# Optimization experiments

Hardware: AMD Instinct MI355X
Metric: run time of the kernel (lower is better)

## Reference

```python
import jax, jax.numpy as jnp
import numpy as np

HEADS = 4

def _proj(x, w, b):
    # 1x1 conv == per-pixel linear: x [B,C,H,W], w [O,C], b [O]
    return jnp.einsum('oc,bchw->bohw', w, x) + b[None, :, None, None]

def setup_inputs() -> dict:
    key = jax.random.key(0)
    ks = jax.random.split(key, 9)
    B, C, H, W = 16, 512, 32, 32
    emb = C // HEADS
    return {
        'x': jax.random.normal(ks[0], (B, C, H, W), jnp.float32),
        'wq_w': jax.random.normal(ks[1], (C, C), jnp.float32) * 0.02,
        'wq_b': jax.random.normal(ks[2], (C,), jnp.float32) * 0.02,
        'wk_w': jax.random.normal(ks[3], (C, C), jnp.float32) * 0.02,
        'wk_b': jax.random.normal(ks[4], (C,), jnp.float32) * 0.02,
        'wv_w': jax.random.normal(ks[5], (C, C), jnp.float32) * 0.02,
        'wv_b': jax.random.normal(ks[6], (C,), jnp.float32) * 0.02,
        'rh': jax.random.normal(ks[7], (1, HEADS, emb, 1, H), jnp.float32),
        'rw': jax.random.normal(ks[8], (1, HEADS, emb, W, 1), jnp.float32),
    }

def reference(x, wq_w, wq_b, wk_w, wk_b, wv_w, wv_b, rh, rw):
    B, C, H, W = x.shape
    heads = HEADS
    emb = C // heads
    scale = C ** (-0.5)
    N = H * W
    q = _proj(x, wq_w, wq_b).reshape(B, heads, emb, N).transpose(0, 1, 3, 2) * scale  # [B,h,N,d]
    kt = _proj(x, wk_w, wk_b).reshape(B, heads, emb, N)                               # [B,h,d,N]
    v = _proj(x, wv_w, wv_b).reshape(B, heads, emb, N).transpose(0, 1, 3, 2)          # [B,h,N,d]
    qkt = jnp.matmul(q, kt)                                                           # [B,h,N,N]
    # relative-position term: (rh + rw) broadcasts to [1,h,d,W,H], flattened as in source
    rt = (rh + rw).reshape(1, heads, emb, N)
    qrt = jnp.matmul(q, rt)                                                           # [B,h,N,N]
    attn = jax.nn.softmax(qkt + qrt, axis=-1)
    y = jnp.matmul(attn, v)                                                           # [B,h,N,d]
    return y.reshape(B, C, H, W)
```

## Files before the change

### kernel.cpp

```cpp
#include <hip/hip_runtime.h>
#include <hip/hip_bf16.h>
#include <cstdint>

#define NB 16
#define NC 512
#define NPIX 1024
#define NHEADS 4
#define NEMB 128

typedef short bf16x8 __attribute__((ext_vector_type(8)));
typedef float f32x4 __attribute__((ext_vector_type(4)));
typedef float f32x16 __attribute__((ext_vector_type(16)));
typedef unsigned short u16x4 __attribute__((ext_vector_type(4)));
typedef unsigned short u16x8 __attribute__((ext_vector_type(8)));

__device__ __forceinline__ unsigned short f2bf(float f) {
  union { float f; unsigned u; } c; c.f = f;
  return (unsigned short)((c.u + 0x7FFFu + ((c.u >> 16) & 1u)) >> 16);
}

__device__ __forceinline__ unsigned cvtpk_bf16(float lo, float hi) {
  unsigned r;
  asm("v_cvt_pk_bf16_f32 %0, %1, %2" : "=v"(r) : "v"(lo), "v"(hi));
  return r;
}

__device__ __forceinline__ void gload_lds16(const void* g, void* l) {
  __builtin_amdgcn_global_load_lds(
      (const __attribute__((address_space(1))) unsigned int*)g,
      (__attribute__((address_space(3))) unsigned int*)l, 16, 0, 0);
}

__global__ void k_prep_x(const float* __restrict__ x, unsigned short* __restrict__ xt) {
  __shared__ float tile[4][32][33];
  int bid = blockIdx.x;
  int nt = bid & 31, ct4 = (bid >> 5) & 3, b = bid >> 7;
  int n0 = nt * 32, c0 = ct4 * 128;
  int t = threadIdx.x;
  int r = t >> 3, q = t & 7;
#pragma unroll
  for (int s = 0; s < 4; s++) {
    float4 v = *(const float4*)(x + ((size_t)(b * NC + c0 + s * 32 + r)) * NPIX + n0 + q * 4);
    tile[s][r][q * 4 + 0] = v.x; tile[s][r][q * 4 + 1] = v.y;
    tile[s][r][q * 4 + 2] = v.z; tile[s][r][q * 4 + 3] = v.w;
  }
  __syncthreads();
  int cl = q * 4;
#pragma unroll
  for (int s = 0; s < 4; s++) {
    u16x4 o;
    o[0] = f2bf(tile[s][cl + 0][r]); o[1] = f2bf(tile[s][cl + 1][r]);
    o[2] = f2bf(tile[s][cl + 2][r]); o[3] = f2bf(tile[s][cl + 3][r]);
    *(u16x4*)(xt + ((size_t)(b * NPIX + n0 + r)) * NC + c0 + s * 32 + cl) = o;
  }
}

__global__ void k_prep_w(const float* __restrict__ wq, const float* __restrict__ wk,
                         const float* __restrict__ wv, unsigned short* __restrict__ wb) {
  const float* src = blockIdx.y == 0 ? wq : (blockIdx.y == 1 ? wk : wv);
  unsigned short* dst = wb + (size_t)blockIdx.y * NC * NC;
  for (int i = blockIdx.x * 256 + threadIdx.x; i < NC * NC / 4; i += gridDim.x * 256) {
    float4 v = ((const float4*)src)[i];
    u16x4 o = { f2bf(v.x), f2bf(v.y), f2bf(v.z), f2bf(v.w) };
    ((u16x4*)dst)[i] = o;
  }
}

__global__ __launch_bounds__(256, 3) void k_qkv(
    const unsigned short* __restrict__ wb, const unsigned short* __restrict__ xt,
    const float* __restrict__ qb, const float* __restrict__ kb, const float* __restrict__ vb,
    const float* __restrict__ rh, const float* __restrict__ rw,
    unsigned short* __restrict__ Qs, unsigned short* __restrict__ Kn,
    unsigned short* __restrict__ Vm) {
  __shared__ unsigned short Alds[128 * 64];
  __shared__ unsigned short Blds[128 * 64];
  int bid = blockIdx.x;
  int nt = bid & 7, mt = (bid >> 3) & 3;
  int rest = bid >> 5;
  int p = rest % 3, b = rest / 3;
  int m0 = mt * 128, n0 = nt * 128;
  const unsigned short* A = wb + (size_t)p * NC * NC + (size_t)m0 * NC;
  const unsigned short* Bx = xt + (size_t)b * NPIX * NC + (size_t)n0 * NC;
  int t = threadIdx.x;
  int lane = t & 63, wid = t >> 6;
  int wm = (wid >> 1) * 64, wn = (wid & 1) * 64;
  f32x4 acc[4][4] = {};
  for (int k0 = 0; k0 < NC; k0 += 64) {
#pragma unroll
    for (int i = 0; i < 4; i++) {
      int idx = i * 256 + t;
      int row = idx >> 3, col = (idx & 7) * 8;
      gload_lds16(A + (size_t)row * NC + k0 + col, &Alds[idx * 8]);
    }
#pragma unroll
    for (int i = 0; i < 4; i++) {
      int idx = i * 256 + t;
      int row = idx >> 3, col = (idx & 7) * 8;
      gload_lds16(Bx + (size_t)row * NC + k0 + col, &Blds[idx * 8]);
    }
    __syncthreads();
#pragma unroll
    for (int ks = 0; ks < 2; ks++) {
      int kk = ks * 32 + ((lane >> 4) << 3);
      bf16x8 af[4], bfr[4];
#pragma unroll
      for (int f = 0; f < 4; f++)
        af[f] = *(const bf16x8*)&Alds[(wm + f * 16 + (lane & 15)) * 64 + kk];
#pragma unroll
      for (int f = 0; f < 4; f++)
        bfr[f] = *(const bf16x8*)&Blds[(wn + f * 16 + (lane & 15)) * 64 + kk];
#pragma unroll
      for (int fm = 0; fm < 4; fm++)
#pragma unroll
        for (int fn = 0; fn < 4; fn++)
          acc[fm][fn] = __builtin_amdgcn_mfma_f32_16x16x32_bf16(af[fm], bfr[fn], acc[fm][fn], 0, 0, 0);
    }
    __syncthreads();
  }
  const float scale = 0.044194173824159216f * 1.4426950408889634f;
  if (p == 2) {
    unsigned short* vbase = Vm + (size_t)(b * NHEADS + mt) * 131072;
#pragma unroll
    for (int fm = 0; fm < 4; fm++) {
#pragma unroll
      for (int r = 0; r < 4; r++) {
        int d = wm + fm * 16 + ((lane >> 4) << 2) + r;
        float bv = vb[m0 + d];
#pragma unroll
        for (int fn = 0; fn < 4; fn++) {
          int j = n0 + wn + fn * 16 + (lane & 15);
          int tile = j >> 6, jl = j & 63;
          int c2 = jl >> 4, h5 = (jl >> 3) & 1, j8 = jl & 7;
          size_t flat = ((((size_t)tile * 4 + c2) * 2 + h5) * 128 + d) * 8 + j8;
          vbase[flat] = f2bf(acc[fm][fn][r] + bv);
        }
      }
    }
  } else if (p == 1) {
    unsigned short* kbase = Kn + (size_t)(b * NHEADS + mt) * 131072;
#pragma unroll
    for (int fm = 0; fm < 4; fm++) {
      int e0 = wm + fm * 16 + ((lane >> 4) << 2);
      int d8 = e0 >> 4, h5 = (e0 >> 3) & 1, e8 = e0 & 7;
#pragma unroll
      for (int fn = 0; fn < 4; fn++) {
        int j = n0 + wn + fn * 16 + (lane & 15);
        int tile = j >> 6, jl = j & 63;
        u16x4 o;
#pragma unroll
        for (int r = 0; r < 4; r++) {
          float v = acc[fm][fn][r] + kb[m0 + e0 + r];
          v += rh[(m0 + e0 + r) * 32 + (j & 31)] + rw[(m0 + e0 + r) * 32 + (j >> 5)];
          o[r] = f2bf(v);
        }
        size_t flat = ((((size_t)tile * 8 + d8) * 2 + h5) * 64 + jl) * 8 + e8;
        *(u16x4*)(kbase + flat) = o;
      }
    }
  } else {
    unsigned short* dst = Qs + ((size_t)((b * NHEADS + mt) * NPIX + n0)) * NEMB;
#pragma unroll
    for (int fm = 0; fm < 4; fm++) {
      int e0 = wm + fm * 16 + ((lane >> 4) << 2);
#pragma unroll
      for (int fn = 0; fn < 4; fn++) {
        int ncol = wn + fn * 16 + (lane & 15);
        u16x4 o;
#pragma unroll
        for (int r = 0; r < 4; r++)
          o[r] = f2bf((acc[fm][fn][r] + qb[m0 + e0 + r]) * scale);
        *(u16x4*)&dst[(size_t)ncol * NEMB + e0] = o;
      }
    }
  }
}

__global__ __launch_bounds__(256, 2) void k_attn(
    const unsigned short* __restrict__ Qs, const unsigned short* __restrict__ Kp,
    const unsigned short* __restrict__ Vp, float* __restrict__ out) {
  int bid = blockIdx.x;
  int pair = bid & 63;
  int b = pair >> 2, hd = pair & 3;
  int i0 = (bid >> 6) * 128;
  int t = threadIdx.x, w = t >> 6, lane = t & 63;
  int l31 = lane & 31, hi5 = lane >> 5;
  const unsigned short* Qb = Qs + (size_t)pair * NPIX * NEMB;
  const unsigned short* Kg = Kp + (size_t)pair * 131072;
  const unsigned short* Vg = Vp + (size_t)pair * 131072;

  bf16x8 qf[8];
  {
    const unsigned short* qr = Qb + (size_t)(i0 + w * 32 + l31) * NEMB + hi5 * 8;
#pragma unroll
    for (int d8 = 0; d8 < 8; d8++) qf[d8] = *(const bf16x8*)(qr + d8 * 16);
  }
  f32x16 yacc[4] = {};
  float l = 0.f;

  for (int tt = 0; tt < 16; tt++) {
    bf16x8 kf0[8], kf1[8];
#pragma unroll
    for (int d8 = 0; d8 < 8; d8++) {
      const unsigned short* kp = Kg + (((size_t)tt * 8 + d8) * 2 + hi5) * 512;
      kf0[d8] = *(const bf16x8*)(kp + l31 * 8);
      kf1[d8] = *(const bf16x8*)(kp + (l31 + 32) * 8);
    }
    f32x16 sacc[2] = {};
    __builtin_amdgcn_s_setprio(1);
#pragma unroll
    for (int d8 = 0; d8 < 8; d8++) {
      sacc[0] = __builtin_amdgcn_mfma_f32_32x32x16_bf16(kf0[d8], qf[d8], sacc[0], 0, 0, 0);
      sacc[1] = __builtin_amdgcn_mfma_f32_32x32x16_bf16(kf1[d8], qf[d8], sacc[1], 0, 0, 0);
    }
    __builtin_amdgcn_s_setprio(0);
    bf16x8 vf[4][4];
#pragma unroll
    for (int c2 = 0; c2 < 4; c2++)
#pragma unroll
      for (int ds = 0; ds < 4; ds++)
        vf[c2][ds] = *(const bf16x8*)(
            Vg + ((((size_t)tt * 4 + c2) * 2 + hi5) * 128 + ds * 32 + l31) * 8);
    float rs0 = 0.f, rs1 = 0.f, rs2 = 0.f, rs3 = 0.f;
#pragma unroll
    for (int c = 0; c < 2; c++)
#pragma unroll
      for (int i = 0; i < 16; i += 4) {
        float p0 = exp2f(sacc[c][i + 0]);
        float p1 = exp2f(sacc[c][i + 1]);
        float p2 = exp2f(sacc[c][i + 2]);
        float p3 = exp2f(sacc[c][i + 3]);
        sacc[c][i + 0] = p0; sacc[c][i + 1] = p1;
        sacc[c][i + 2] = p2; sacc[c][i + 3] = p3;
        rs0 += p0; rs1 += p1; rs2 += p2; rs3 += p3;
      }
    l += (rs0 + rs1) + (rs2 + rs3);
    unsigned up[2][4][2];
#pragma unroll
    for (int c = 0; c < 2; c++)
#pragma unroll
      for (int g = 0; g < 4; g++) {
        up[c][g][0] = cvtpk_bf16(sacc[c][4 * g + 0], sacc[c][4 * g + 1]);
        up[c][g][1] = cvtpk_bf16(sacc[c][4 * g + 2], sacc[c][4 * g + 3]);
      }
    bf16x8 pf[4];
#pragma unroll
    for (int c2 = 0; c2 < 4; c2++) {
      int c = c2 >> 1, gA = (c2 & 1) * 2, gB = gA + 1;
      unsigned a0 = up[c][gA][0], b0 = up[c][gB][0];
      unsigned a1 = up[c][gA][1], b1 = up[c][gB][1];
      asm("v_permlane32_swap_b32 %0, %1" : "+v"(a0), "+v"(b0));
      asm("v_permlane32_swap_b32 %0, %1" : "+v"(a1), "+v"(b1));
      unsigned wd[4] = { a0, a1, b0, b1 };
      pf[c2] = *(bf16x8*)wd;
    }
    __builtin_amdgcn_s_setprio(1);
#pragma unroll
    for (int c2 = 0; c2 < 4; c2++)
#pragma unroll
      for (int ds = 0; ds < 4; ds++)
        yacc[ds] = __builtin_amdgcn_mfma_f32_32x32x16_bf16(vf[c2][ds], pf[c2], yacc[ds], 0, 0, 0);
    __builtin_amdgcn_s_setprio(0);
  }
  float ltot = l + __shfl_xor(l, 32);
  float invl = 1.0f / ltot;
  int q = i0 + w * 32 + l31;
  float* orow = out + ((size_t)(b * NC + hd * NEMB + (q >> 3))) * NPIX + (q & 7) * NEMB;
#pragma unroll
  for (int ds = 0; ds < 4; ds++)
#pragma unroll
    for (int rg = 0; rg < 4; rg++) {
      f32x4 v;
#pragma unroll
      for (int i = 0; i < 4; i++) v[i] = yacc[ds][rg * 4 + i] * invl;
      *(f32x4*)(orow + ds * 32 + rg * 8 + hi5 * 4) = v;
    }
}

extern "C" void kernel_launch(void* const* d_in, const int* in_sizes, int n_in,
                              void* d_out, int out_size, void* d_ws, size_t ws_size,
                              hipStream_t stream) {
  const float* x  = (const float*)d_in[0];
  const float* wq = (const float*)d_in[1];
  const float* qb = (const float*)d_in[2];
  const float* wk = (const float*)d_in[3];
  const float* kb = (const float*)d_in[4];
  const float* wv = (const float*)d_in[5];
  const float* vb = (const float*)d_in[6];
  const float* rh = (const float*)d_in[7];
  const float* rw = (const float*)d_in[8];
  float* out = (float*)d_out;
  char* ws = (char*)d_ws;
  unsigned short* xt = (unsigned short*)(ws);
  unsigned short* wb = (unsigned short*)(ws + 16777216);
  unsigned short* Q  = (unsigned short*)(ws + 18350080);
  unsigned short* K  = (unsigned short*)(ws + 35127296);
  unsigned short* V  = (unsigned short*)(ws + 51904512);
  k_prep_x<<<2048, 256, 0, stream>>>(x, xt);
  k_prep_w<<<dim3(64, 3), 256, 0, stream>>>(wq, wk, wv, wb);
  k_qkv<<<1536, 256, 0, stream>>>(wb, xt, qb, kb, vb, rh, rw, Q, K, V);
  k_attn<<<512, 256, 0, stream>>>(Q, K, V, out);
}
```

Baseline: 107.6 us.

## Stage K tiles in swizzled LDS with double-buffered async global-to-LDS loads

The K projection now writes its output in a row-major, XOR-swizzled byte layout. The attention kernel streams each 64-key K tile into a 32KB double-buffered LDS area with direct global-to-LDS loads, prefetching the next tile while the current one is consumed. Each block therefore loads a K tile from global memory once and shares it across its four waves, instead of every wave reading it from L2 into registers. The swizzle is meant to avoid LDS bank conflicts. The cost is a block-wide barrier every iteration and more LDS use, which could limit occupancy or add stalls.

```diff
diff --git a/kernel.cpp b/kernel.cpp
--- a/kernel.cpp
+++ b/kernel.cpp
@@ -137,11 +137,10 @@
       }
     }
   } else if (p == 1) {
-    unsigned short* kbase = Kn + (size_t)(b * NHEADS + mt) * 131072;
+    char* kbase = (char*)(Kn + (size_t)(b * NHEADS + mt) * 16 * 8192);
 #pragma unroll
     for (int fm = 0; fm < 4; fm++) {
       int e0 = wm + fm * 16 + ((lane >> 4) << 2);
-      int d8 = e0 >> 4, h5 = (e0 >> 3) & 1, e8 = e0 & 7;
 #pragma unroll
       for (int fn = 0; fn < 4; fn++) {
         int j = n0 + wn + fn * 16 + (lane & 15);
@@ -153,8 +152,7 @@
           v += rh[(m0 + e0 + r) * 32 + (j & 31)] + rw[(m0 + e0 + r) * 32 + (j >> 5)];
           o[r] = f2bf(v);
         }
-        size_t flat = ((((size_t)tile * 8 + d8) * 2 + h5) * 64 + jl) * 8 + e8;
-        *(u16x4*)(kbase + flat) = o;
+        *(u16x4*)(kbase + tile * 16384 + jl * 256 + ((2 * e0) ^ ((jl & 7) << 4))) = o;
       }
     }
   } else {
@@ -178,6 +176,7 @@
 __global__ __launch_bounds__(256, 2) void k_attn(
     const unsigned short* __restrict__ Qs, const unsigned short* __restrict__ Kp,
     const unsigned short* __restrict__ Vp, float* __restrict__ out) {
+  __shared__ __align__(16) char smem[32768];
   int bid = blockIdx.x;
   int pair = bid & 63;
   int b = pair >> 2, hd = pair & 3;
@@ -185,7 +184,7 @@
   int t = threadIdx.x, w = t >> 6, lane = t & 63;
   int l31 = lane & 31, hi5 = lane >> 5;
   const unsigned short* Qb = Qs + (size_t)pair * NPIX * NEMB;
-  const unsigned short* Kg = Kp + (size_t)pair * 131072;
+  const char* Kpb = (const char*)(Kp + (size_t)pair * 16 * 8192);
   const unsigned short* Vg = Vp + (size_t)pair * 131072;
 
   bf16x8 qf[8];
@@ -197,22 +196,35 @@
   f32x16 yacc[4] = {};
   float l = 0.f;
 
+#pragma unroll
+  for (int r = 0; r < 4; r++)
+    gload_lds16(Kpb + r * 4096 + t * 16, smem + r * 4096 + t * 16);
+  __syncthreads();
+
   for (int tt = 0; tt < 16; tt++) {
-    bf16x8 kf0[8], kf1[8];
-#pragma unroll
-    for (int d8 = 0; d8 < 8; d8++) {
-      const unsigned short* kp = Kg + (((size_t)tt * 8 + d8) * 2 + hi5) * 512;
-      kf0[d8] = *(const bf16x8*)(kp + l31 * 8);
-      kf1[d8] = *(const bf16x8*)(kp + (l31 + 32) * 8);
-    }
+    int cur = tt & 1;
+    if (tt < 15) {
+      const char* kn = Kpb + (tt + 1) * 16384;
+      char* kd = smem + (cur ^ 1) * 16384;
+#pragma unroll
+      for (int r = 0; r < 4; r++)
+        gload_lds16(kn + r * 4096 + t * 16, kd + r * 4096 + t * 16);
+    }
+    const char* Kl = smem + cur * 16384;
     f32x16 sacc[2] = {};
-    __builtin_amdgcn_s_setprio(1);
-#pragma unroll
-    for (int d8 = 0; d8 < 8; d8++) {
-      sacc[0] = __builtin_amdgcn_mfma_f32_32x32x16_bf16(kf0[d8], qf[d8], sacc[0], 0, 0, 0);
-      sacc[1] = __builtin_amdgcn_mfma_f32_32x32x16_bf16(kf1[d8], qf[d8], sacc[1], 0, 0, 0);
-    }
-    __builtin_amdgcn_s_setprio(0);
+    {
+      int swz = (l31 & 7) << 4;
+#pragma unroll
+      for (int d8 = 0; d8 < 8; d8++) {
+        int colb = (d8 * 32 + hi5 * 16) ^ swz;
+        bf16x8 k0 = *(const bf16x8*)(Kl + l31 * 256 + colb);
+        bf16x8 k1 = *(const bf16x8*)(Kl + (32 + l31) * 256 + colb);
+        __builtin_amdgcn_s_setprio(1);
+        sacc[0] = __builtin_amdgcn_mfma_f32_32x32x16_bf16(k0, qf[d8], sacc[0], 0, 0, 0);
+        sacc[1] = __builtin_amdgcn_mfma_f32_32x32x16_bf16(k1, qf[d8], sacc[1], 0, 0, 0);
+        __builtin_amdgcn_s_setprio(0);
+      }
+    }
     bf16x8 vf[4][4];
 #pragma unroll
     for (int c2 = 0; c2 < 4; c2++)
@@ -260,6 +272,7 @@
       for (int ds = 0; ds < 4; ds++)
         yacc[ds] = __builtin_amdgcn_mfma_f32_32x32x16_bf16(vf[c2][ds], pf[c2], yacc[ds], 0, 0, 0);
     __builtin_amdgcn_s_setprio(0);
+    __syncthreads();
   }
   float ltot = l + __shfl_xor(l, 32);
   float invl = 1.0f / ltot;
```

After: 109.2 us. About the same (+1.5%).
